# Kernel tuning notes

Measured on AMD Instinct MI355X. Metric: run time of the kernel, lower is better.

## Reference

```python
import jax, jax.numpy as jnp
import numpy as np

N, E = 50000, 800000
F_IN, HID, HEADS, OUT = 128, 32, 4, 16
NEG_SLOPE = 0.2  # PyG GATConv default leaky_relu slope


def segment_softmax(logits, seg, n):
    # numerically stable softmax over edges grouped by destination node
    m = jax.ops.segment_max(logits, seg, num_segments=n)          # [N,H]
    m = jnp.where(jnp.isfinite(m), m, 0.0)                        # guard empty segments
    e = jnp.exp(logits - m[seg])                                  # [E,H]
    s = jax.ops.segment_sum(e, seg, num_segments=n)               # [N,H]
    return e / (s[seg] + 1e-16)


def gat_conv(x, W, a_src, a_dst, bias, src, dst, concat):
    H, C = a_src.shape
    n = x.shape[0]
    h = (x @ W).reshape(n, H, C)                                  # [N,H,C]
    alpha_src = jnp.einsum('nhc,hc->nh', h, a_src)                # [N,H]
    alpha_dst = jnp.einsum('nhc,hc->nh', h, a_dst)                # [N,H]
    e = jax.nn.leaky_relu(alpha_src[src] + alpha_dst[dst], NEG_SLOPE)  # [E,H]
    alpha = segment_softmax(e, dst, n)                            # [E,H]
    msg = h[src] * alpha[:, :, None]                              # [E,H,C]
    out = jax.ops.segment_sum(msg, dst, num_segments=n)           # [N,H,C]
    out = out.reshape(n, H * C) if concat else out.mean(axis=1)
    return out + bias


def setup_inputs() -> dict:
    key = jax.random.key(0)
    ks = jax.random.split(key, 12)
    s = 0.1  # keep attention logits in a sane range
    return {
        'x': jax.random.normal(ks[0], (N, F_IN), jnp.float32),
        'edge_index': jax.random.randint(ks[1], (2, E), 0, N),
        'Wemb': jax.random.normal(ks[2], (F_IN, HID), jnp.float32) * s,
        'bemb': jnp.zeros((HID,), jnp.float32),
        'W1': jax.random.normal(ks[3], (HID, HEADS * HID), jnp.float32) * s,
        'a_src1': jax.random.normal(ks[4], (HEADS, HID), jnp.float32) * s,
        'a_dst1': jax.random.normal(ks[5], (HEADS, HID), jnp.float32) * s,
        'b1': jnp.zeros((HEADS * HID,), jnp.float32),
        'W2': jax.random.normal(ks[6], (HEADS * HID, HEADS * OUT), jnp.float32) * s,
        'a_src2': jax.random.normal(ks[7], (HEADS, OUT), jnp.float32) * s,
        'a_dst2': jax.random.normal(ks[8], (HEADS, OUT), jnp.float32) * s,
        'b2': jnp.zeros((OUT,), jnp.float32),
    }


def reference(x, edge_index, Wemb, bemb, W1, a_src1, a_dst1, b1, W2, a_src2, a_dst2, b2):
    src, dst = edge_index[0], edge_index[1]
    h = x @ Wemb + bemb  # dropout layers are identity at inference
    h = jax.nn.elu(gat_conv(h, W1, a_src1, a_dst1, b1, src, dst, True))
    h = gat_conv(h, W2, a_src2, a_dst2, b2, src, dst, False)
    return jax.nn.log_softmax(h, axis=1)
```

## Files before the change

### kernel.cpp

```cpp
#include <hip/hip_runtime.h>

#define N_NODES 50000
#define N_EDGES 800000
#define F_IN    128
#define HID     32
#define HEADS   4
#define OUT_C   16

#define NBKT 196
#define CAP  5120
#define EPB  4096
#define NB64 782

typedef __attribute__((ext_vector_type(8))) short bf16x8;
typedef __attribute__((ext_vector_type(4))) float f32x4;

__device__ __forceinline__ unsigned short f2bf(float f) {
    unsigned int u = __float_as_uint(f);
    u += 0x7FFFu + ((u >> 16) & 1u);
    return (unsigned short)(u >> 16);
}
__device__ __forceinline__ float bf_lo(unsigned int u) { return __uint_as_float(u << 16); }
__device__ __forceinline__ float bf_hi(unsigned int u) { return __uint_as_float(u & 0xFFFF0000u); }
__device__ __forceinline__ float bf2f(unsigned short s) {
    return __uint_as_float(((unsigned int)s) << 16);
}

__device__ __forceinline__ float edge_w(float asv, float adv) {
    float v = asv + adv;
    v = (v > 0.f) ? v : 0.2f * v;
    return __expf(v);
}

__global__ __launch_bounds__(256) void k_F1(const float* __restrict__ x,
                                            const float* __restrict__ Wemb,
                                            const float* __restrict__ bemb,
                                            float* __restrict__ h0,
                                            const int* __restrict__ ei,
                                            int* __restrict__ gcnt,
                                            unsigned int* __restrict__ pairs) {
    __shared__ float xs[64][132];
    __shared__ float Wl[F_IN][HID];
    __shared__ float bl[HID];
    __shared__ int hist[NBKT];
    __shared__ int base[NBKT];
    int t = threadIdx.x;
    if (blockIdx.x < NB64) {
        int node0 = blockIdx.x * 64;
        if (t < HID) bl[t] = bemb[t];
        #pragma unroll
        for (int it = 0; it < 4; it++) {
            int idx = it * 256 + t;
            *(float4*)((float*)Wl + idx * 4) = *(const float4*)(Wemb + idx * 4);
        }
        #pragma unroll
        for (int it = 0; it < 8; it++) {
            int idx = it * 256 + t;
            int row = idx >> 5, c4 = idx & 31;
            float4 v = make_float4(0.f, 0.f, 0.f, 0.f);
            if (node0 + row < N_NODES) v = *(const float4*)(x + (size_t)(node0 + row) * F_IN + c4 * 4);
            *(float4*)&xs[row][c4 * 4] = v;
        }
        __syncthreads();
        int c = t & 7, g = t >> 3;
        float acc[2][4] = {};
        for (int k = 0; k < F_IN; k++) {
            float4 w4 = *(const float4*)&Wl[k][c * 4];
            #pragma unroll
            for (int n = 0; n < 2; n++) {
                float xv = xs[g * 2 + n][k];
                acc[n][0] += xv * w4.x; acc[n][1] += xv * w4.y;
                acc[n][2] += xv * w4.z; acc[n][3] += xv * w4.w;
            }
        }
        #pragma unroll
        for (int n = 0; n < 2; n++) {
            int node = node0 + g * 2 + n;
            if (node < N_NODES) {
                float4 o = make_float4(acc[n][0] + bl[c * 4], acc[n][1] + bl[c * 4 + 1],
                                       acc[n][2] + bl[c * 4 + 2], acc[n][3] + bl[c * 4 + 3]);
                *(float4*)(h0 + (size_t)node * HID + c * 4) = o;
            }
        }
    } else {
        int e0 = (blockIdx.x - NB64) * EPB;
        for (int i = t; i < NBKT; i += 256) hist[i] = 0;
        __syncthreads();
        unsigned int p[16];
        int bb[16];
        #pragma unroll
        for (int i = 0; i < 16; i++) {
            int e = e0 + i * 256 + t;
            bb[i] = -1;
            if (e < N_EDGES) {
                int s = ei[e], d = ei[N_EDGES + e];
                p[i] = ((unsigned int)s << 8) | (unsigned int)(d & 255);
                bb[i] = d >> 8;
                atomicAdd(&hist[bb[i]], 1);
            }
        }
        __syncthreads();
        for (int i = t; i < NBKT; i += 256) {
            int c = hist[i];
            base[i] = i * CAP + (c ? atomicAdd(&gcnt[i], c) : 0);
            hist[i] = 0;
        }
        __syncthreads();
        #pragma unroll
        for (int i = 0; i < 16; i++) {
            if (bb[i] >= 0) {
                int off = atomicAdd(&hist[bb[i]], 1);
                pairs[base[bb[i]] + off] = p[i];
            }
        }
    }
}

__global__ __launch_bounds__(256) void k_F2(const float* __restrict__ h0,
                                            const float* __restrict__ W1,
                                            const float* __restrict__ a_src,
                                            const float* __restrict__ a_dst,
                                            unsigned short* __restrict__ h1,
                                            float* __restrict__ as, float* __restrict__ ad,
                                            const unsigned int* __restrict__ pairs,
                                            const int* __restrict__ gcnt,
                                            int* __restrict__ rowptr,
                                            int* __restrict__ esrc) {
    __shared__ float xs[64][36];
    __shared__ float Wl[HID][128];
    __shared__ int cnt[256];
    __shared__ int cur[256];
    __shared__ int wsum[4];
    int t = threadIdx.x;
    if (blockIdx.x < NB64) {
        int node0 = blockIdx.x * 64;
        #pragma unroll
        for (int it = 0; it < 4; it++) {
            int idx = it * 256 + t;
            *(float4*)((float*)Wl + idx * 4) = *(const float4*)(W1 + idx * 4);
        }
        #pragma unroll
        for (int it = 0; it < 2; it++) {
            int idx = it * 256 + t;
            int row = idx >> 3, c4 = idx & 7;
            float4 v = make_float4(0.f, 0.f, 0.f, 0.f);
            if (node0 + row < N_NODES) v = *(const float4*)(h0 + (size_t)(node0 + row) * HID + c4 * 4);
            *(float4*)&xs[row][c4 * 4] = v;
        }
        __syncthreads();
        int c = t & 31, g = t >> 5;
        float acc[8][4] = {};
        for (int k = 0; k < HID; k++) {
            float4 w4 = *(const float4*)&Wl[k][c * 4];
            #pragma unroll
            for (int n = 0; n < 8; n++) {
                float xv = xs[g * 8 + n][k];
                acc[n][0] += xv * w4.x; acc[n][1] += xv * w4.y;
                acc[n][2] += xv * w4.z; acc[n][3] += xv * w4.w;
            }
        }
        float4 av = *(const float4*)(a_src + c * 4);
        float4 dv = *(const float4*)(a_dst + c * 4);
        float ps[8], pd[8];
        #pragma unroll
        for (int n = 0; n < 8; n++) {
            int node = node0 + g * 8 + n;
            if (node < N_NODES) {
                ushort4 o;
                o.x = f2bf(acc[n][0]); o.y = f2bf(acc[n][1]);
                o.z = f2bf(acc[n][2]); o.w = f2bf(acc[n][3]);
                *(ushort4*)(h1 + (size_t)node * 128 + c * 4) = o;
            }
            ps[n] = acc[n][0] * av.x + acc[n][1] * av.y + acc[n][2] * av.z + acc[n][3] * av.w;
            pd[n] = acc[n][0] * dv.x + acc[n][1] * dv.y + acc[n][2] * dv.z + acc[n][3] * dv.w;
        }
        #pragma unroll
        for (int mask = 1; mask <= 4; mask <<= 1) {
            #pragma unroll
            for (int n = 0; n < 8; n++) {
                ps[n] += __shfl_xor(ps[n], mask, 64);
                pd[n] += __shfl_xor(pd[n], mask, 64);
            }
        }
        if ((c & 7) == 0) {
            int hh = c >> 3;
            #pragma unroll
            for (int n = 0; n < 8; n++) {
                int node = node0 + g * 8 + n;
                if (node < N_NODES) { as[node * 4 + hh] = ps[n]; ad[node * 4 + hh] = pd[n]; }
            }
        }
    } else {
        int b = blockIdx.x - NB64;
        int lane = t & 63, wv = t >> 6;
        int v0 = (t < NBKT && t < b) ? gcnt[t] : 0;
        #pragma unroll
        for (int mask = 1; mask < 64; mask <<= 1) v0 += __shfl_xor(v0, mask, 64);
        if (lane == 0) wsum[wv] = v0;
        __syncthreads();
        int base = wsum[0] + wsum[1] + wsum[2] + wsum[3];
        int n0 = b << 8;
        int cntb = gcnt[b];
        int s0 = b * CAP;
        cnt[t] = 0;
        __syncthreads();
        for (int i = t; i < cntb; i += 256) atomicAdd(&cnt[pairs[s0 + i] & 255], 1);
        __syncthreads();
        int v = cnt[t], x = v;
        #pragma unroll
        for (int off = 1; off < 64; off <<= 1) { int y = __shfl_up(x, off, 64); if (lane >= off) x += y; }
        __syncthreads();
        if (lane == 63) wsum[wv] = x;
        __syncthreads();
        int add = 0;
        for (int j = 0; j < wv; j++) add += wsum[j];
        int excl = base + (x - v) + add;
        cur[t] = excl;
        if (n0 + t < N_NODES) rowptr[n0 + t] = excl;
        if (b == 0 && t == 0) rowptr[N_NODES] = N_EDGES;
        __syncthreads();
        for (int i = t; i < cntb; i += 256) {
            unsigned int p = pairs[s0 + i];
            int pos = atomicAdd(&cur[p & 255], 1);
            esrc[pos] = (int)(p >> 8);
        }
    }
}

__global__ __launch_bounds__(256) void k_h2f(const unsigned int* __restrict__ hin,
                                             const float* __restrict__ W2,
                                             const float* __restrict__ a_src,
                                             const float* __restrict__ a_dst,
                                             unsigned short* __restrict__ h2,
                                             float* __restrict__ as, float* __restrict__ ad) {
    __shared__ unsigned int xsu[64][68];
    __shared__ unsigned short w2t[64][136];
    int t = threadIdx.x;
    int node0 = blockIdx.x * 64;
    #pragma unroll
    for (int it = 0; it < 4; it++) {
        int idx = it * 256 + t;
        int row = idx >> 4, c4 = idx & 15;
        uint4 v = make_uint4(0u, 0u, 0u, 0u);
        if (node0 + row < N_NODES) v = *(const uint4*)(hin + (size_t)(node0 + row) * 64 + c4 * 4);
        *(uint4*)&xsu[row][c4 * 4] = v;
    }
    #pragma unroll
    for (int it = 0; it < 8; it++) {
        int idx = it * 256 + t;
        int k = idx >> 4, n4 = idx & 15;
        float4 w = *(const float4*)(W2 + k * 64 + n4 * 4);
        w2t[n4 * 4 + 0][k] = f2bf(w.x);
        w2t[n4 * 4 + 1][k] = f2bf(w.y);
        w2t[n4 * 4 + 2][k] = f2bf(w.z);
        w2t[n4 * 4 + 3][k] = f2bf(w.w);
    }
    __syncthreads();
    int lane = t & 63, wv = t >> 6;
    int lrow = lane & 15, lk = lane >> 4;
    f32x4 acc[4] = {};
    const char* xbase = (const char*)&xsu[wv * 16 + lrow][0] + lk * 16;
    #pragma unroll
    for (int kt = 0; kt < 4; kt++) {
        bf16x8 af = *(const bf16x8*)(xbase + kt * 64);
        #pragma unroll
        for (int h = 0; h < 4; h++) {
            bf16x8 bfr = *(const bf16x8*)((const char*)&w2t[h * 16 + lrow][0] + kt * 64 + lk * 16);
            acc[h] = __builtin_amdgcn_mfma_f32_16x16x32_bf16(af, bfr, acc[h], 0, 0, 0);
        }
    }
    float av[4], dv[4];
    #pragma unroll
    for (int h = 0; h < 4; h++) { av[h] = a_src[h * 16 + lrow]; dv[h] = a_dst[h * 16 + lrow]; }
    #pragma unroll
    for (int r = 0; r < 4; r++) {
        int node = node0 + wv * 16 + lk * 4 + r;
        float psh[4], pdh[4];
        #pragma unroll
        for (int h = 0; h < 4; h++) {
            float v = acc[h][r];
            if (node < N_NODES) h2[(size_t)node * 64 + h * 16 + lrow] = f2bf(v);
            float p = v * av[h], q = v * dv[h];
            #pragma unroll
            for (int mask = 1; mask < 16; mask <<= 1) {
                p += __shfl_xor(p, mask, 64);
                q += __shfl_xor(q, mask, 64);
            }
            psh[h] = p; pdh[h] = q;
        }
        if (lrow == 0 && node < N_NODES) {
            *(float4*)(as + node * 4) = make_float4(psh[0], psh[1], psh[2], psh[3]);
            *(float4*)(ad + node * 4) = make_float4(pdh[0], pdh[1], pdh[2], pdh[3]);
        }
    }
}

__global__ __launch_bounds__(256) void k_gather1(const int* __restrict__ esrc,
                                                 const int* __restrict__ rowptr,
                                                 const unsigned int* __restrict__ h1,
                                                 const float* __restrict__ as,
                                                 const float* __restrict__ ad,
                                                 const float* __restrict__ b1,
                                                 unsigned int* __restrict__ out1) {
    int t = threadIdx.x;
    int node = blockIdx.x * 4 + (t >> 6);
    int lane = t & 63;
    int head = lane >> 4;
    int s16 = lane >> 2;
    int h4 = lane & 3;
    int lb = lane * 4;
    int hb = head * 4;
    int beg = rowptr[node], end = rowptr[node + 1];
    float ad_w = ad[node * 4 + h4];
    float ax = 0.f, ay = 0.f, s = 0.f;
    const char* h1c = (const char*)h1;
    for (int k = beg; k < end; k += 16) {
        int idx = k + s16;
        int sm = esrc[min(idx, end - 1)];
#define G1L(J) int sj##J = __builtin_amdgcn_readlane(sm, (J) * 4); \
        unsigned int u##J = *(const unsigned int*)(h1c + (size_t)(unsigned)sj##J * 256 + lb);
        G1L(0)  G1L(1)  G1L(2)  G1L(3)  G1L(4)  G1L(5)  G1L(6)  G1L(7)
        G1L(8)  G1L(9)  G1L(10) G1L(11) G1L(12) G1L(13) G1L(14) G1L(15)
#undef G1L
        float wm = edge_w(as[sm * 4 + h4], ad_w);
        if (idx >= end) wm = 0.f;
        int wmi = __float_as_int(wm);
#define G1W(J) float w##J = __int_as_float(__builtin_amdgcn_ds_bpermute(hb + (J) * 16, wmi));
        G1W(0)  G1W(1)  G1W(2)  G1W(3)  G1W(4)  G1W(5)  G1W(6)  G1W(7)
        G1W(8)  G1W(9)  G1W(10) G1W(11) G1W(12) G1W(13) G1W(14) G1W(15)
#undef G1W
        ax += bf_lo(u0)  * w0  + bf_lo(u1)  * w1  + bf_lo(u2)  * w2  + bf_lo(u3)  * w3
            + bf_lo(u4)  * w4  + bf_lo(u5)  * w5  + bf_lo(u6)  * w6  + bf_lo(u7)  * w7
            + bf_lo(u8)  * w8  + bf_lo(u9)  * w9  + bf_lo(u10) * w10 + bf_lo(u11) * w11
            + bf_lo(u12) * w12 + bf_lo(u13) * w13 + bf_lo(u14) * w14 + bf_lo(u15) * w15;
        ay += bf_hi(u0)  * w0  + bf_hi(u1)  * w1  + bf_hi(u2)  * w2  + bf_hi(u3)  * w3
            + bf_hi(u4)  * w4  + bf_hi(u5)  * w5  + bf_hi(u6)  * w6  + bf_hi(u7)  * w7
            + bf_hi(u8)  * w8  + bf_hi(u9)  * w9  + bf_hi(u10) * w10 + bf_hi(u11) * w11
            + bf_hi(u12) * w12 + bf_hi(u13) * w13 + bf_hi(u14) * w14 + bf_hi(u15) * w15;
        s += (w0 + w1 + w2 + w3) + (w4 + w5 + w6 + w7)
           + (w8 + w9 + w10 + w11) + (w12 + w13 + w14 + w15);
    }
    float rs = 1.0f / (s + 1e-16f);
    float2 bv = *(const float2*)(b1 + 2 * lane);
    float vx = ax * rs + bv.x;
    float vy = ay * rs + bv.y;
    vx = (vx > 0.f) ? vx : (__expf(vx) - 1.0f);
    vy = (vy > 0.f) ? vy : (__expf(vy) - 1.0f);
    out1[(size_t)node * 64 + lane] = ((unsigned int)f2bf(vy) << 16) | (unsigned int)f2bf(vx);
}

__global__ __launch_bounds__(256) void k_gather2(const int* __restrict__ esrc,
                                                 const int* __restrict__ rowptr,
                                                 const unsigned short* __restrict__ h2,
                                                 const float* __restrict__ as,
                                                 const float* __restrict__ ad,
                                                 const float* __restrict__ b2,
                                                 float* __restrict__ out) {
    int t = threadIdx.x;
    int node = blockIdx.x * 4 + (t >> 6);
    int lane = t & 63;
    int head = lane >> 4, c = lane & 15;
    int s16 = lane >> 2;
    int h4 = lane & 3;
    int lb = lane * 2;
    int hb = head * 4;
    int beg = rowptr[node], end = rowptr[node + 1];
    float ad_w = ad[node * 4 + h4];
    float acc = 0.f, s = 0.f;
    const char* h2c = (const char*)h2;
    for (int k = beg; k < end; k += 16) {
        int idx = k + s16;
        int sm = esrc[min(idx, end - 1)];
#define G2L(J) int sj##J = __builtin_amdgcn_readlane(sm, (J) * 4); \
        float r##J = bf2f(*(const unsigned short*)(h2c + (size_t)(unsigned)sj##J * 128 + lb));
        G2L(0)  G2L(1)  G2L(2)  G2L(3)  G2L(4)  G2L(5)  G2L(6)  G2L(7)
        G2L(8)  G2L(9)  G2L(10) G2L(11) G2L(12) G2L(13) G2L(14) G2L(15)
#undef G2L
        float wm = edge_w(as[sm * 4 + h4], ad_w);
        if (idx >= end) wm = 0.f;
        int wmi = __float_as_int(wm);
#define G2W(J) float w##J = __int_as_float(__builtin_amdgcn_ds_bpermute(hb + (J) * 16, wmi));
        G2W(0)  G2W(1)  G2W(2)  G2W(3)  G2W(4)  G2W(5)  G2W(6)  G2W(7)
        G2W(8)  G2W(9)  G2W(10) G2W(11) G2W(12) G2W(13) G2W(14) G2W(15)
#undef G2W
        acc += r0 * w0 + r1 * w1 + r2 * w2 + r3 * w3
             + r4 * w4 + r5 * w5 + r6 * w6 + r7 * w7
             + r8 * w8 + r9 * w9 + r10 * w10 + r11 * w11
             + r12 * w12 + r13 * w13 + r14 * w14 + r15 * w15;
        s += (w0 + w1 + w2 + w3) + (w4 + w5 + w6 + w7)
           + (w8 + w9 + w10 + w11) + (w12 + w13 + w14 + w15);
    }
    float v = acc * (1.0f / (s + 1e-16f));
    v += __shfl_xor(v, 16, 64);
    v += __shfl_xor(v, 32, 64);
    v = v * 0.25f + b2[c];
    float m = v;
    #pragma unroll
    for (int mask = 1; mask < 16; mask <<= 1) m = fmaxf(m, __shfl_xor(m, mask, 64));
    float ex = __expf(v - m);
    float se = ex;
    #pragma unroll
    for (int mask = 1; mask < 16; mask <<= 1) se += __shfl_xor(se, mask, 64);
    float res = (v - m) - __logf(se);
    if (lane < 16) out[(size_t)node * 16 + lane] = res;
}

extern "C" void kernel_launch(void* const* d_in, const int* in_sizes, int n_in,
                              void* d_out, int out_size, void* d_ws, size_t ws_size,
                              hipStream_t stream) {
    const float* x      = (const float*)d_in[0];
    const int*   ei     = (const int*)d_in[1];
    const float* Wemb   = (const float*)d_in[2];
    const float* bemb   = (const float*)d_in[3];
    const float* W1     = (const float*)d_in[4];
    const float* a_src1 = (const float*)d_in[5];
    const float* a_dst1 = (const float*)d_in[6];
    const float* b1     = (const float*)d_in[7];
    const float* W2     = (const float*)d_in[8];
    const float* a_src2 = (const float*)d_in[9];
    const float* a_dst2 = (const float*)d_in[10];
    const float* b2     = (const float*)d_in[11];
    float* out = (float*)d_out;

    char* ws = (char*)d_ws;
    size_t off = 0;
    auto alloc = [&](size_t bytes) { char* p = ws + off; off += (bytes + 255) & ~size_t(255); return p; };
    unsigned short* h1b   = (unsigned short*)alloc((size_t)N_NODES * 128 * 2);
    unsigned int*   out1b = (unsigned int*)alloc((size_t)N_NODES * 64 * 4);
    float*        h0    = (float*)alloc((size_t)N_NODES * HID * 4);
    int*          esrc  = (int*)alloc((size_t)N_EDGES * 4 + 64);
    unsigned int* pairs = (unsigned int*)alloc((size_t)NBKT * CAP * 4);
    float* as     = (float*)alloc((size_t)N_NODES * 4 * 4);
    float* ad     = (float*)alloc((size_t)N_NODES * 4 * 4);
    int*   rowptr = (int*)alloc((size_t)(N_NODES + 1) * 4);
    int*   gcnt   = (int*)alloc((size_t)NBKT * 4);
    unsigned short* h2b = h1b;

    const int GB = N_NODES / 4;

    hipMemsetAsync(gcnt, 0, (size_t)NBKT * 4, stream);
    k_F1<<<NB64 + NBKT, 256, 0, stream>>>(x, Wemb, bemb, h0, ei, gcnt, pairs);
    k_F2<<<NB64 + NBKT, 256, 0, stream>>>(h0, W1, a_src1, a_dst1, h1b, as, ad,
                                          pairs, gcnt, rowptr, esrc);
    k_gather1<<<GB, 256, 0, stream>>>(esrc, rowptr, (const unsigned int*)h1b, as, ad, b1, out1b);
    k_h2f<<<NB64, 256, 0, stream>>>((const unsigned int*)out1b, W2, a_src2, a_dst2, h2b, as, ad);
    k_gather2<<<GB, 256, 0, stream>>>(esrc, rowptr, h2b, as, ad, b2, out);
}
```

Before: 204.1 us.

## Aggregate bf16 h0 in layer-1 gather and apply W1 after aggregation

Layer-1 message passing now gathers the 32-wide bf16 embedding h0 per head instead of the 128-wide projected h1. The W1 projection is applied per node after the softmax-weighted sum, which is valid because the projection is linear. This cuts per-edge gather bytes by about four times and removes the h1 write in k_F2. In exchange, every gather block stages W1 into LDS, adds a barrier and a small per-node matmul, and k_F1 writes an extra bf16 copy of h0.

```diff
diff --git a/kernel.cpp b/kernel.cpp
--- a/kernel.cpp
+++ b/kernel.cpp
@@ -36,6 +36,7 @@
                                             const float* __restrict__ Wemb,
                                             const float* __restrict__ bemb,
                                             float* __restrict__ h0,
+                                            unsigned short* __restrict__ h0b,
                                             const int* __restrict__ ei,
                                             int* __restrict__ gcnt,
                                             unsigned int* __restrict__ pairs) {
@@ -80,6 +81,9 @@
                 float4 o = make_float4(acc[n][0] + bl[c * 4], acc[n][1] + bl[c * 4 + 1],
                                        acc[n][2] + bl[c * 4 + 2], acc[n][3] + bl[c * 4 + 3]);
                 *(float4*)(h0 + (size_t)node * HID + c * 4) = o;
+                ushort4 ob;
+                ob.x = f2bf(o.x); ob.y = f2bf(o.y); ob.z = f2bf(o.z); ob.w = f2bf(o.w);
+                *(ushort4*)(h0b + (size_t)node * HID + c * 4) = ob;
             }
         }
     } else {
@@ -120,7 +124,6 @@
                                             const float* __restrict__ W1,
                                             const float* __restrict__ a_src,
                                             const float* __restrict__ a_dst,
-                                            unsigned short* __restrict__ h1,
                                             float* __restrict__ as, float* __restrict__ ad,
                                             const unsigned int* __restrict__ pairs,
                                             const int* __restrict__ gcnt,
@@ -164,13 +167,6 @@
         float ps[8], pd[8];
         #pragma unroll
         for (int n = 0; n < 8; n++) {
-            int node = node0 + g * 8 + n;
-            if (node < N_NODES) {
-                ushort4 o;
-                o.x = f2bf(acc[n][0]); o.y = f2bf(acc[n][1]);
-                o.z = f2bf(acc[n][2]); o.w = f2bf(acc[n][3]);
-                *(ushort4*)(h1 + (size_t)node * 128 + c * 4) = o;
-            }
             ps[n] = acc[n][0] * av.x + acc[n][1] * av.y + acc[n][2] * av.z + acc[n][3] * av.w;
             pd[n] = acc[n][0] * dv.x + acc[n][1] * dv.y + acc[n][2] * dv.z + acc[n][3] * dv.w;
         }
@@ -297,28 +293,37 @@
 
 __global__ __launch_bounds__(256) void k_gather1(const int* __restrict__ esrc,
                                                  const int* __restrict__ rowptr,
-                                                 const unsigned int* __restrict__ h1,
+                                                 const unsigned int* __restrict__ h0b,
                                                  const float* __restrict__ as,
                                                  const float* __restrict__ ad,
+                                                 const float* __restrict__ W1,
                                                  const float* __restrict__ b1,
                                                  unsigned int* __restrict__ out1) {
+    __shared__ float Wl[HID][128];
+    __shared__ float aw[4][4][32];
     int t = threadIdx.x;
+    #pragma unroll
+    for (int it = 0; it < 4; it++) {
+        int idx = it * 256 + t;
+        *(float4*)((float*)Wl + idx * 4) = *(const float4*)(W1 + idx * 4);
+    }
     int node = blockIdx.x * 4 + (t >> 6);
     int lane = t & 63;
     int head = lane >> 4;
+    int cp = lane & 15;
     int s16 = lane >> 2;
     int h4 = lane & 3;
-    int lb = lane * 4;
+    int lb = cp * 4;
     int hb = head * 4;
     int beg = rowptr[node], end = rowptr[node + 1];
     float ad_w = ad[node * 4 + h4];
     float ax = 0.f, ay = 0.f, s = 0.f;
-    const char* h1c = (const char*)h1;
+    const char* hc = (const char*)h0b;
     for (int k = beg; k < end; k += 16) {
         int idx = k + s16;
         int sm = esrc[min(idx, end - 1)];
 #define G1L(J) int sj##J = __builtin_amdgcn_readlane(sm, (J) * 4); \
-        unsigned int u##J = *(const unsigned int*)(h1c + (size_t)(unsigned)sj##J * 256 + lb);
+        unsigned int u##J = *(const unsigned int*)(hc + (size_t)(unsigned)sj##J * 64 + lb);
         G1L(0)  G1L(1)  G1L(2)  G1L(3)  G1L(4)  G1L(5)  G1L(6)  G1L(7)
         G1L(8)  G1L(9)  G1L(10) G1L(11) G1L(12) G1L(13) G1L(14) G1L(15)
 #undef G1L
@@ -341,9 +346,19 @@
            + (w8 + w9 + w10 + w11) + (w12 + w13 + w14 + w15);
     }
     float rs = 1.0f / (s + 1e-16f);
+    int wv = t >> 6;
+    aw[wv][head][cp * 2]     = ax * rs;
+    aw[wv][head][cp * 2 + 1] = ay * rs;
+    __syncthreads();
     float2 bv = *(const float2*)(b1 + 2 * lane);
-    float vx = ax * rs + bv.x;
-    float vy = ay * rs + bv.y;
+    float vx = 0.f, vy = 0.f;
+    #pragma unroll
+    for (int k2 = 0; k2 < HID; k2++) {
+        float a = aw[wv][head][k2];
+        float2 w2 = *(const float2*)&Wl[k2][2 * lane];
+        vx += a * w2.x; vy += a * w2.y;
+    }
+    vx += bv.x; vy += bv.y;
     vx = (vx > 0.f) ? vx : (__expf(vx) - 1.0f);
     vy = (vy > 0.f) ? vy : (__expf(vy) - 1.0f);
     out1[(size_t)node * 64 + lane] = ((unsigned int)f2bf(vy) << 16) | (unsigned int)f2bf(vx);
@@ -425,24 +440,24 @@
     char* ws = (char*)d_ws;
     size_t off = 0;
     auto alloc = [&](size_t bytes) { char* p = ws + off; off += (bytes + 255) & ~size_t(255); return p; };
-    unsigned short* h1b   = (unsigned short*)alloc((size_t)N_NODES * 128 * 2);
+    unsigned short* h2b   = (unsigned short*)alloc((size_t)N_NODES * 64 * 2);
     unsigned int*   out1b = (unsigned int*)alloc((size_t)N_NODES * 64 * 4);
     float*        h0    = (float*)alloc((size_t)N_NODES * HID * 4);
+    unsigned short* h0b = (unsigned short*)alloc((size_t)N_NODES * HID * 2);
     int*          esrc  = (int*)alloc((size_t)N_EDGES * 4 + 64);
     unsigned int* pairs = (unsigned int*)alloc((size_t)NBKT * CAP * 4);
     float* as     = (float*)alloc((size_t)N_NODES * 4 * 4);
     float* ad     = (float*)alloc((size_t)N_NODES * 4 * 4);
     int*   rowptr = (int*)alloc((size_t)(N_NODES + 1) * 4);
     int*   gcnt   = (int*)alloc((size_t)NBKT * 4);
-    unsigned short* h2b = h1b;
 
     const int GB = N_NODES / 4;
 
     hipMemsetAsync(gcnt, 0, (size_t)NBKT * 4, stream);
-    k_F1<<<NB64 + NBKT, 256, 0, stream>>>(x, Wemb, bemb, h0, ei, gcnt, pairs);
-    k_F2<<<NB64 + NBKT, 256, 0, stream>>>(h0, W1, a_src1, a_dst1, h1b, as, ad,
+    k_F1<<<NB64 + NBKT, 256, 0, stream>>>(x, Wemb, bemb, h0, h0b, ei, gcnt, pairs);
+    k_F2<<<NB64 + NBKT, 256, 0, stream>>>(h0, W1, a_src1, a_dst1, as, ad,
                                           pairs, gcnt, rowptr, esrc);
-    k_gather1<<<GB, 256, 0, stream>>>(esrc, rowptr, (const unsigned int*)h1b, as, ad, b1, out1b);
+    k_gather1<<<GB, 256, 0, stream>>>(esrc, rowptr, (const unsigned int*)h0b, as, ad, W1, b1, out1b);
     k_h2f<<<NB64, 256, 0, stream>>>((const unsigned int*)out1b, W2, a_src2, a_dst2, h2b, as, ad);
     k_gather2<<<GB, 256, 0, stream>>>(esrc, rowptr, h2b, as, ad, b2, out);
 }
```

Measured after the change: 198.4 us. 2.8% less time.
